# Kernel tuning notes

Measured on AMD Instinct MI355X. Metric: run time of the kernel, lower is better.

## Reference

```python
import jax, jax.numpy as jnp
import numpy as np

H = 16
D_MODEL = 1024
D_K = D_MODEL // H


def setup_inputs() -> dict:
    key = jax.random.key(0)
    ks = jax.random.split(key, 12)
    B, S = 2, 2048
    scale = 1.0 / np.sqrt(D_MODEL)
    inp = {
        "query": jax.random.normal(ks[0], (B, S, D_MODEL), jnp.float32),
        "key": jax.random.normal(ks[1], (B, S, D_MODEL), jnp.float32),
        "value": jax.random.normal(ks[2], (B, S, D_MODEL), jnp.float32),
        "mask": jnp.ones((B, 1, S), jnp.int32),
        "Wq": jax.random.normal(ks[3], (D_MODEL, D_MODEL), jnp.float32) * scale,
        "bq": jnp.zeros((D_MODEL,), jnp.float32),
        "Wk": jax.random.normal(ks[4], (D_MODEL, D_MODEL), jnp.float32) * scale,
        "bk": jnp.zeros((D_MODEL,), jnp.float32),
        "Wv": jax.random.normal(ks[5], (D_MODEL, D_MODEL), jnp.float32) * scale,
        "bv": jnp.zeros((D_MODEL,), jnp.float32),
        "Wo": jax.random.normal(ks[6], (D_MODEL, D_MODEL), jnp.float32) * scale,
        "bo": jnp.zeros((D_MODEL,), jnp.float32),
    }
    return inp


def reference(query, key, value, mask, Wq, bq, Wk, bk, Wv, bv, Wo, bo):
    B, S, _ = query.shape
    # QKV projections, split heads: [B, S, D] -> [B, H, S, d_k]
    def proj(x, W, b):
        y = x @ W.T + b
        return y.reshape(B, -1, H, D_K).transpose(0, 2, 1, 3)

    q = proj(query, Wq, bq)
    k = proj(key, Wk, bk)
    v = proj(value, Wv, bv)

    # scaled dot-product attention with full score matrix [B, H, Sq, Sk]
    scores = jnp.einsum("bhqd,bhkd->bhqk", q, k) / np.sqrt(D_K)
    m = mask[:, None, :, :]  # unsqueeze head dim: [B, 1, 1_or_S, S]
    scores = jnp.where(m == 0, jnp.float32(-1e9), scores)
    p_attn = jax.nn.softmax(scores, axis=-1)  # dropout p=0.0 (eval)
    x = jnp.einsum("bhqk,bhkd->bhqd", p_attn, v)

    # merge heads and output projection
    x = x.transpose(0, 2, 1, 3).reshape(B, -1, H * D_K)
    return x @ Wo.T + bo
```

## Files before the change

kernel.cpp:

```cpp
#include <hip/hip_runtime.h>
#include <hip/hip_bf16.h>
#include <stdint.h>

typedef unsigned short us;
typedef __bf16 bf8 __attribute__((ext_vector_type(8)));
typedef float  f4  __attribute__((ext_vector_type(4)));

typedef unsigned int __attribute__((address_space(1))) as1_uint;
typedef unsigned int __attribute__((address_space(3))) as3_uint;

__device__ __forceinline__ void async_ld16(const void* g, void* l) {
    __builtin_amdgcn_global_load_lds((as1_uint*)g, (as3_uint*)l, 16, 0, 0);
}

__device__ __forceinline__ us f2bf(float f) {
    __hip_bfloat16 h = __float2bfloat16(f);
    us u;
    __builtin_memcpy(&u, &h, 2);
    return u;
}

__global__ __launch_bounds__(256)
void convert_all(const float* __restrict__ s0, const float* __restrict__ s1,
                 const float* __restrict__ s2, const float* __restrict__ s3,
                 const float* __restrict__ s4, const float* __restrict__ s5,
                 const float* __restrict__ s6,
                 us* __restrict__ d0, us* __restrict__ d1, us* __restrict__ d2,
                 us* __restrict__ d3, us* __restrict__ d4, us* __restrict__ d5,
                 us* __restrict__ d6)
{
    size_t i4 = (((size_t)blockIdx.x * 256) + threadIdx.x) << 2;
    const float* src; us* dst; size_t off;
    if (i4 < ((size_t)3 << 22)) {
        unsigned seg = (unsigned)(i4 >> 22);
        off = i4 & (((size_t)1 << 22) - 1);
        src = seg == 0 ? s0 : (seg == 1 ? s1 : s2);
        dst = seg == 0 ? d0 : (seg == 1 ? d1 : d2);
    } else {
        size_t j = i4 - ((size_t)3 << 22);
        unsigned seg = (unsigned)(j >> 20);
        off = j & (((size_t)1 << 20) - 1);
        src = seg == 0 ? s3 : (seg == 1 ? s4 : (seg == 2 ? s5 : s6));
        dst = seg == 0 ? d3 : (seg == 1 ? d4 : (seg == 2 ? d5 : d6));
    }
    float4 f = *(const float4*)(src + off);
    ushort4 o;
    o.x = f2bf(f.x); o.y = f2bf(f.y); o.z = f2bf(f.z); o.w = f2bf(f.w);
    *(ushort4*)(dst + off) = o;
}

template<int MODE, int BN>
__device__ __forceinline__
void gemm_body(const us* __restrict__ A, const us* __restrict__ W,
               const float* __restrict__ bias, void* __restrict__ out,
               float scale, int bx, int by)
{
    __shared__ us lA[128 * 32];
    __shared__ us lB[BN * 32];

    const int tid  = threadIdx.x;
    const int wv   = tid >> 6;
    const int lane = tid & 63;
    const int l15  = lane & 15;
    const int quad = lane >> 4;
    const int kq   = quad << 3;
    const int cr   = quad << 2;
    const int srow = lane >> 2;
    const int scol = (lane & 3) << 3;
    const int m0   = by << 7;
    const int n0   = bx * BN;
    constexpr int MJ = (BN == 128) ? 4 : 2;
    const int wm = (BN == 128) ? ((wv >> 1) << 6) : (wv << 5);
    const int wn = (BN == 128) ? ((wv & 1) << 6) : 0;

    f4 acc[4][MJ];
    const f4 zero = {0.f, 0.f, 0.f, 0.f};
#pragma unroll
    for (int i = 0; i < 4; ++i)
#pragma unroll
        for (int j = 0; j < MJ; ++j) acc[i][j] = zero;

    for (int kt = 0; kt < 1024; kt += 32) {
#pragma unroll
        for (int s = 0; s < 2; ++s) {
            const int chunk = wv * 2 + s;
            const int row   = chunk * 16 + srow;
            async_ld16(A + (size_t)(m0 + row) * 1024 + kt + scol, &lA[chunk * 512]);
        }
        if (BN == 128) {
#pragma unroll
            for (int s = 0; s < 2; ++s) {
                const int chunk = wv * 2 + s;
                const int row   = chunk * 16 + srow;
                async_ld16(W + (size_t)(n0 + row) * 1024 + kt + scol, &lB[chunk * 512]);
            }
        } else {
            const int row = wv * 16 + srow;
            async_ld16(W + (size_t)(n0 + row) * 1024 + kt + scol, &lB[wv * 512]);
        }
        __syncthreads();

        bf8 wf[4], xf[MJ];
#pragma unroll
        for (int i = 0; i < 4; ++i)
            wf[i] = *(const bf8*)&lB[(wn + i * 16 + l15) * 32 + kq];
#pragma unroll
        for (int j = 0; j < MJ; ++j)
            xf[j] = *(const bf8*)&lA[(wm + j * 16 + l15) * 32 + kq];
#pragma unroll
        for (int i = 0; i < 4; ++i)
#pragma unroll
            for (int j = 0; j < MJ; ++j)
                acc[i][j] = __builtin_amdgcn_mfma_f32_16x16x32_bf16(wf[i], xf[j], acc[i][j], 0, 0, 0);
        __syncthreads();
    }

#pragma unroll
    for (int i = 0; i < 4; ++i) {
        const int gnb = n0 + wn + i * 16 + cr;
        const f4 bj = *(const f4*)&bias[gnb];
        if (MODE == 0) {
            us* o = (us*)out;
            const int hh = gnb >> 6, dd = gnb & 63;
#pragma unroll
            for (int j = 0; j < MJ; ++j) {
                const int gm = m0 + wm + j * 16 + l15;
                const int bb = gm >> 11, ss = gm & 2047;
                us hp[4];
#pragma unroll
                for (int r = 0; r < 4; ++r)
                    hp[r] = f2bf((acc[i][j][r] + bj[r]) * scale);
                uint2 w;
                w.x = (unsigned)hp[0] | ((unsigned)hp[1] << 16);
                w.y = (unsigned)hp[2] | ((unsigned)hp[3] << 16);
                *(uint2*)&o[(((size_t)(bb * 16 + hh) * 2048 + ss) << 6) + dd] = w;
            }
        } else {
            float* o = (float*)out;
#pragma unroll
            for (int j = 0; j < MJ; ++j) {
                const int gm = m0 + wm + j * 16 + l15;
                f4 v;
#pragma unroll
                for (int r = 0; r < 4; ++r) v[r] = acc[i][j][r] + bj[r];
                *(f4*)&o[((size_t)gm << 10) + gnb] = v;
            }
        }
    }
}

__global__ __launch_bounds__(256)
void gemm_qkv(const us* __restrict__ XQ, const us* __restrict__ XK,
              const us* __restrict__ XV,
              const us* __restrict__ WQ, const us* __restrict__ WK,
              const us* __restrict__ WV,
              const float* __restrict__ bq, const float* __restrict__ bk,
              const float* __restrict__ bv,
              us* __restrict__ QP, us* __restrict__ KP, us* __restrict__ VP)
{
    const int z = blockIdx.z;
    const us* A = z == 0 ? XQ : (z == 1 ? XK : XV);
    const us* W = z == 0 ? WQ : (z == 1 ? WK : WV);
    const float* b = z == 0 ? bq : (z == 1 ? bk : bv);
    us* o = z == 0 ? QP : (z == 1 ? KP : VP);
    const float scale = z == 0 ? 0.125f : 1.0f;
    gemm_body<0, 128>(A, W, b, o, scale, blockIdx.x, blockIdx.y);
}

__global__ __launch_bounds__(256)
void gemm_o(const us* __restrict__ A, const us* __restrict__ W,
            const float* __restrict__ bias, float* __restrict__ out)
{
    gemm_body<1, 64>(A, W, bias, out, 1.0f, blockIdx.x, blockIdx.y);
}

__global__ __launch_bounds__(256)
void flash_attn(const us* __restrict__ Qp, const us* __restrict__ Kp,
                const us* __restrict__ Vp, const int* __restrict__ maskp,
                us* __restrict__ ctx)
{
    __shared__ char smem[27136];
    us* lK    = (us*)smem;
    us* lVt   = (us*)(smem + 8192);
    us* lP    = (us*)(smem + 16384);
    float* lmask = (float*)(smem + 26624);
    float* liRed = (float*)(smem + 26880);
    float* red   = (float*)smem;

    const int tid  = threadIdx.x;
    const int wv   = tid >> 6;
    const int lane = tid & 63;
    const int l15  = lane & 15;
    const int quad = lane >> 4;
    const int cr   = quad << 2;
    const int qh   = wv & 1;
    const int kh   = wv >> 1;

    const int q0 = blockIdx.x << 6;
    const int h  = blockIdx.y;
    const int b  = blockIdx.z;

    const size_t headoff = ((size_t)(b * 16 + h)) << 17;
    const us* Qh = Qp + headoff;
    const us* Kh = Kp + headoff;
    const us* Vh = Vp + headoff;

    bf8 qf[2][2];
#pragma unroll
    for (int nt = 0; nt < 2; ++nt)
#pragma unroll
        for (int kb = 0; kb < 2; ++kb)
            qf[nt][kb] = *(const bf8*)(Qh + ((size_t)(q0 + qh * 32 + nt * 16 + l15) << 6)
                                          + kb * 32 + (quad << 3));

    const f4 zero = {0.f, 0.f, 0.f, 0.f};
    f4 of[4][2];
#pragma unroll
    for (int mt = 0; mt < 4; ++mt)
#pragma unroll
        for (int nt = 0; nt < 2; ++nt) of[mt][nt] = zero;
    float li[2] = {0.f, 0.f};

    us* lPw = lP + wv * (32 * 40);
    const int sc = tid & 7;
    const int sr = tid >> 3;
    const int ls = lane >> 3;

    for (int kt0 = 0; kt0 < 2048; kt0 += 64) {
        __syncthreads();

#pragma unroll
        for (int it = 0; it < 2; ++it) {
            const int r = sr + 32 * it;
            uint4 kv = *(const uint4*)(Kh + ((size_t)(kt0 + r) << 6) + sc * 8);
            *(uint4*)&lK[r * 64 + ((sc ^ ls) << 3)] = kv;
        }
#pragma unroll
        for (int it = 0; it < 2; ++it) {
            const int r = sr + 32 * it;
            uint4 vv = *(const uint4*)(Vh + ((size_t)(kt0 + r) << 6) + sc * 8);
            const us* u = (const us*)&vv;
            const int rhi = r >> 3;
#pragma unroll
            for (int jj = 0; jj < 8; ++jj) {
                const int d = sc * 8 + jj;
                const int p = (rhi ^ jj ^ sc) & 7;
                lVt[d * 64 + (p << 3) + ls] = u[jj];
            }
        }
        if (tid < 64)
            lmask[tid] = (maskp[((size_t)b << 11) + kt0 + tid] == 0) ? 0.0f : 1.0f;
        __syncthreads();

        f4 st[2][2];
#pragma unroll
        for (int mt2 = 0; mt2 < 2; ++mt2)
#pragma unroll
            for (int nt = 0; nt < 2; ++nt) st[mt2][nt] = zero;
#pragma unroll
        for (int mt2 = 0; mt2 < 2; ++mt2) {
            const int key = kh * 32 + mt2 * 16 + l15;
#pragma unroll
            for (int kb = 0; kb < 2; ++kb) {
                const int c = 4 * kb + quad;
                bf8 kf = *(const bf8*)&lK[key * 64 + ((c ^ (l15 & 7)) << 3)];
#pragma unroll
                for (int nt = 0; nt < 2; ++nt)
                    st[mt2][nt] = __builtin_amdgcn_mfma_f32_16x16x32_bf16(kf, qf[nt][kb], st[mt2][nt], 0, 0, 0);
            }
        }

        float rs[2] = {0.f, 0.f};
#pragma unroll
        for (int mt2 = 0; mt2 < 2; ++mt2) {
            const f4 mr = *(const f4*)&lmask[kh * 32 + mt2 * 16 + cr];
#pragma unroll
            for (int nt = 0; nt < 2; ++nt) {
                us hp[4];
#pragma unroll
                for (int r = 0; r < 4; ++r) {
                    const float pv = __expf(st[mt2][nt][r]) * mr[r];
                    rs[nt] += pv;
                    hp[r] = f2bf(pv);
                }
                uint2 w;
                w.x = (unsigned)hp[0] | ((unsigned)hp[1] << 16);
                w.y = (unsigned)hp[2] | ((unsigned)hp[3] << 16);
                *(uint2*)&lPw[(nt * 16 + l15) * 40 + mt2 * 16 + cr] = w;
            }
        }
#pragma unroll
        for (int nt = 0; nt < 2; ++nt) {
            float r2 = rs[nt];
            r2 += __shfl_xor(r2, 16, 64);
            r2 += __shfl_xor(r2, 32, 64);
            li[nt] += r2;
        }

        bf8 pf[2];
#pragma unroll
        for (int nt = 0; nt < 2; ++nt)
            pf[nt] = *(const bf8*)&lPw[(nt * 16 + l15) * 40 + (quad << 3)];
#pragma unroll
        for (int mt = 0; mt < 4; ++mt) {
            const int dd = mt * 16 + l15;
            const int c  = 4 * kh + quad;
            const int p  = (c ^ (dd & 7) ^ ((dd >> 3) & 7)) & 7;
            bf8 vf = *(const bf8*)&lVt[dd * 64 + (p << 3)];
#pragma unroll
            for (int nt = 0; nt < 2; ++nt)
                of[mt][nt] = __builtin_amdgcn_mfma_f32_16x16x32_bf16(vf, pf[nt], of[mt][nt], 0, 0, 0);
        }
    }

    __syncthreads();
    if (kh == 1) {
#pragma unroll
        for (int mt = 0; mt < 4; ++mt)
#pragma unroll
            for (int nt = 0; nt < 2; ++nt)
#pragma unroll
                for (int r = 0; r < 4; ++r)
                    red[qh * 2048 + (mt * 16 + cr + r) * 32 + nt * 16 + l15] = of[mt][nt][r];
        if (quad == 0) {
#pragma unroll
            for (int nt = 0; nt < 2; ++nt)
                liRed[qh * 32 + nt * 16 + l15] = li[nt];
        }
    }
    __syncthreads();
    if (kh == 0) {
#pragma unroll
        for (int mt = 0; mt < 4; ++mt)
#pragma unroll
            for (int nt = 0; nt < 2; ++nt)
#pragma unroll
                for (int r = 0; r < 4; ++r)
                    of[mt][nt][r] += red[qh * 2048 + (mt * 16 + cr + r) * 32 + nt * 16 + l15];
#pragma unroll
        for (int nt = 0; nt < 2; ++nt) {
            const float linv = 1.0f / (li[nt] + liRed[qh * 32 + nt * 16 + l15]);
            const int tok = q0 + qh * 32 + nt * 16 + l15;
            const size_t rowb = (((size_t)b * 2048 + tok) << 10) + (h << 6);
#pragma unroll
            for (int mt = 0; mt < 4; ++mt) {
                us hp[4];
#pragma unroll
                for (int r = 0; r < 4; ++r) hp[r] = f2bf(of[mt][nt][r] * linv);
                uint2 w;
                w.x = (unsigned)hp[0] | ((unsigned)hp[1] << 16);
                w.y = (unsigned)hp[2] | ((unsigned)hp[3] << 16);
                *(uint2*)&ctx[rowb + mt * 16 + cr] = w;
            }
        }
    }
}

extern "C" void kernel_launch(void* const* d_in, const int* in_sizes, int n_in,
                              void* d_out, int out_size, void* d_ws, size_t ws_size,
                              hipStream_t stream)
{
    const float* q    = (const float*)d_in[0];
    const float* k    = (const float*)d_in[1];
    const float* v    = (const float*)d_in[2];
    const int*   mask = (const int*)d_in[3];
    const float* Wq   = (const float*)d_in[4];
    const float* bq   = (const float*)d_in[5];
    const float* Wk   = (const float*)d_in[6];
    const float* bk   = (const float*)d_in[7];
    const float* Wv   = (const float*)d_in[8];
    const float* bv   = (const float*)d_in[9];
    const float* Wo   = (const float*)d_in[10];
    const float* bo   = (const float*)d_in[11];
    float* out = (float*)d_out;

    us* ws  = (us*)d_ws;
    us* XQ  = ws;
    us* XK  = ws + 4194304;
    us* XV  = ws + 8388608;
    us* WQb = ws + 12582912;
    us* WKb = ws + 13631488;
    us* WVb = ws + 14680064;
    us* WOb = ws + 15728640;
    us* QP  = ws + 16777216;
    us* KP  = ws + 20971520;
    us* VP  = ws + 25165824;
    us* CTX = XQ;

    convert_all<<<16384, 256, 0, stream>>>(q, k, v, Wq, Wk, Wv, Wo,
                                           XQ, XK, XV, WQb, WKb, WVb, WOb);
    gemm_qkv<<<dim3(8, 32, 3), 256, 0, stream>>>(XQ, XK, XV, WQb, WKb, WVb,
                                                 bq, bk, bv, QP, KP, VP);
    flash_attn<<<dim3(32, 16, 2), 256, 0, stream>>>(QP, KP, VP, mask, CTX);
    gemm_o<<<dim3(16, 32), 256, 0, stream>>>(CTX, WOb, bo, out);
}
```

Before: 272.2 us.

## Emit transposed V from projection GEMM and restructure flash attention per-wave tiling

The V projection is now computed as W·Xᵀ and written directly in a head-major transposed layout, so the attention kernel copies V tiles into LDS with plain vector stores instead of a scalar transpose scatter. The attention kernel moves to 128 threads where each wave owns 64 query rows across the full key tile, which removes the cross-wave output reduction through LDS and raises MFMA work per LDS load. The Q scale now includes log2(e) so a raw exp2 builtin replaces __expf. Fewer, larger blocks reduce total waves in flight, and the higher per-wave register use may lower occupancy.

```diff
diff --git a/kernel.cpp b/kernel.cpp
--- a/kernel.cpp
+++ b/kernel.cpp
@@ -19,6 +19,16 @@
     __builtin_memcpy(&u, &h, 2);
     return u;
 }
+
+__device__ __forceinline__ float fexp2(float x) {
+#if __has_builtin(__builtin_amdgcn_exp2f)
+    return __builtin_amdgcn_exp2f(x);
+#else
+    return exp2f(x);
+#endif
+}
+
+#define SCALE_Q 0.18033688011112042f
 
 __global__ __launch_bounds__(256)
 void convert_all(const float* __restrict__ s0, const float* __restrict__ s1,
@@ -115,6 +125,29 @@
         __syncthreads();
     }
 
+    if (MODE == 2) {
+        us* o = (us*)out;
+#pragma unroll
+        for (int j = 0; j < MJ; ++j) {
+            const int f = m0 + wm + j * 16 + l15;
+            const float bf_ = bias[f];
+            const int hh = f >> 6, dd = f & 63;
+#pragma unroll
+            for (int i = 0; i < 4; ++i) {
+                const int tokb = n0 + wn + i * 16 + cr;
+                const int bb = tokb >> 11, ss = tokb & 2047;
+                us hp[4];
+#pragma unroll
+                for (int r = 0; r < 4; ++r) hp[r] = f2bf(acc[i][j][r] + bf_);
+                uint2 w;
+                w.x = (unsigned)hp[0] | ((unsigned)hp[1] << 16);
+                w.y = (unsigned)hp[2] | ((unsigned)hp[3] << 16);
+                *(uint2*)&o[((size_t)((bb * 16 + hh) * 64 + dd) << 11) + ss] = w;
+            }
+        }
+        return;
+    }
+
 #pragma unroll
     for (int i = 0; i < 4; ++i) {
         const int gnb = n0 + wn + i * 16 + cr;
@@ -156,14 +189,18 @@
               const us* __restrict__ WV,
               const float* __restrict__ bq, const float* __restrict__ bk,
               const float* __restrict__ bv,
-              us* __restrict__ QP, us* __restrict__ KP, us* __restrict__ VP)
+              us* __restrict__ QP, us* __restrict__ KP, us* __restrict__ VT)
 {
     const int z = blockIdx.z;
-    const us* A = z == 0 ? XQ : (z == 1 ? XK : XV);
-    const us* W = z == 0 ? WQ : (z == 1 ? WK : WV);
-    const float* b = z == 0 ? bq : (z == 1 ? bk : bv);
-    us* o = z == 0 ? QP : (z == 1 ? KP : VP);
-    const float scale = z == 0 ? 0.125f : 1.0f;
+    if (z == 2) {
+        gemm_body<2, 128>(WV, XV, bv, VT, 1.0f, blockIdx.y, blockIdx.x);
+        return;
+    }
+    const us* A = z == 0 ? XQ : XK;
+    const us* W = z == 0 ? WQ : WK;
+    const float* b = z == 0 ? bq : bk;
+    us* o = z == 0 ? QP : KP;
+    const float scale = z == 0 ? SCALE_Q : 1.0f;
     gemm_body<0, 128>(A, W, b, o, scale, blockIdx.x, blockIdx.y);
 }
 
@@ -174,18 +211,15 @@
     gemm_body<1, 64>(A, W, bias, out, 1.0f, blockIdx.x, blockIdx.y);
 }
 
-__global__ __launch_bounds__(256)
+__global__ __launch_bounds__(128)
 void flash_attn(const us* __restrict__ Qp, const us* __restrict__ Kp,
-                const us* __restrict__ Vp, const int* __restrict__ maskp,
+                const us* __restrict__ Vtp, const int* __restrict__ maskp,
                 us* __restrict__ ctx)
 {
-    __shared__ char smem[27136];
-    us* lK    = (us*)smem;
-    us* lVt   = (us*)(smem + 8192);
-    us* lP    = (us*)(smem + 16384);
-    float* lmask = (float*)(smem + 26624);
-    float* liRed = (float*)(smem + 26880);
-    float* red   = (float*)smem;
+    __shared__ us lK[64 * 64];
+    __shared__ us lVt[64 * 64];
+    __shared__ us lP[2 * 64 * 72];
+    __shared__ float lmask[64];
 
     const int tid  = threadIdx.x;
     const int wv   = tid >> 6;
@@ -193,165 +227,120 @@
     const int l15  = lane & 15;
     const int quad = lane >> 4;
     const int cr   = quad << 2;
-    const int qh   = wv & 1;
-    const int kh   = wv >> 1;
-
-    const int q0 = blockIdx.x << 6;
+    const int l7   = l15 & 7;
+
+    const int q0 = blockIdx.x << 7;
     const int h  = blockIdx.y;
     const int b  = blockIdx.z;
 
     const size_t headoff = ((size_t)(b * 16 + h)) << 17;
-    const us* Qh = Qp + headoff;
-    const us* Kh = Kp + headoff;
-    const us* Vh = Vp + headoff;
-
-    bf8 qf[2][2];
-#pragma unroll
-    for (int nt = 0; nt < 2; ++nt)
+    const us* Qh  = Qp  + headoff;
+    const us* Kh  = Kp  + headoff;
+    const us* Vth = Vtp + headoff;
+
+    bf8 qf[4][2];
+#pragma unroll
+    for (int nt = 0; nt < 4; ++nt)
 #pragma unroll
         for (int kb = 0; kb < 2; ++kb)
-            qf[nt][kb] = *(const bf8*)(Qh + ((size_t)(q0 + qh * 32 + nt * 16 + l15) << 6)
+            qf[nt][kb] = *(const bf8*)(Qh + ((size_t)(q0 + wv * 64 + nt * 16 + l15) << 6)
                                           + kb * 32 + (quad << 3));
 
     const f4 zero = {0.f, 0.f, 0.f, 0.f};
-    f4 of[4][2];
-#pragma unroll
-    for (int mt = 0; mt < 4; ++mt)
-#pragma unroll
-        for (int nt = 0; nt < 2; ++nt) of[mt][nt] = zero;
-    float li[2] = {0.f, 0.f};
-
-    us* lPw = lP + wv * (32 * 40);
+    f4 of[4][4];
+#pragma unroll
+    for (int dt = 0; dt < 4; ++dt)
+#pragma unroll
+        for (int nt = 0; nt < 4; ++nt) of[dt][nt] = zero;
+    float li[4] = {0.f, 0.f, 0.f, 0.f};
+
+    us* lPw = lP + wv * (64 * 72);
+
+    const int sr = tid >> 3;
     const int sc = tid & 7;
-    const int sr = tid >> 3;
-    const int ls = lane >> 3;
 
     for (int kt0 = 0; kt0 < 2048; kt0 += 64) {
         __syncthreads();
 
 #pragma unroll
-        for (int it = 0; it < 2; ++it) {
-            const int r = sr + 32 * it;
+        for (int it = 0; it < 4; ++it) {
+            const int r = sr + 16 * it;
+            const int sw = (sc ^ (r & 7)) << 3;
             uint4 kv = *(const uint4*)(Kh + ((size_t)(kt0 + r) << 6) + sc * 8);
-            *(uint4*)&lK[r * 64 + ((sc ^ ls) << 3)] = kv;
-        }
-#pragma unroll
-        for (int it = 0; it < 2; ++it) {
-            const int r = sr + 32 * it;
-            uint4 vv = *(const uint4*)(Vh + ((size_t)(kt0 + r) << 6) + sc * 8);
-            const us* u = (const us*)&vv;
-            const int rhi = r >> 3;
-#pragma unroll
-            for (int jj = 0; jj < 8; ++jj) {
-                const int d = sc * 8 + jj;
-                const int p = (rhi ^ jj ^ sc) & 7;
-                lVt[d * 64 + (p << 3) + ls] = u[jj];
-            }
+            *(uint4*)&lK[(r << 6) + sw] = kv;
+            uint4 vv = *(const uint4*)(Vth + (size_t)r * 2048 + kt0 + sc * 8);
+            *(uint4*)&lVt[(r << 6) + sw] = vv;
         }
         if (tid < 64)
             lmask[tid] = (maskp[((size_t)b << 11) + kt0 + tid] == 0) ? 0.0f : 1.0f;
         __syncthreads();
 
-        f4 st[2][2];
-#pragma unroll
-        for (int mt2 = 0; mt2 < 2; ++mt2)
-#pragma unroll
-            for (int nt = 0; nt < 2; ++nt) st[mt2][nt] = zero;
-#pragma unroll
-        for (int mt2 = 0; mt2 < 2; ++mt2) {
-            const int key = kh * 32 + mt2 * 16 + l15;
-#pragma unroll
-            for (int kb = 0; kb < 2; ++kb) {
-                const int c = 4 * kb + quad;
-                bf8 kf = *(const bf8*)&lK[key * 64 + ((c ^ (l15 & 7)) << 3)];
-#pragma unroll
-                for (int nt = 0; nt < 2; ++nt)
-                    st[mt2][nt] = __builtin_amdgcn_mfma_f32_16x16x32_bf16(kf, qf[nt][kb], st[mt2][nt], 0, 0, 0);
-            }
-        }
-
-        float rs[2] = {0.f, 0.f};
-#pragma unroll
-        for (int mt2 = 0; mt2 < 2; ++mt2) {
-            const f4 mr = *(const f4*)&lmask[kh * 32 + mt2 * 16 + cr];
-#pragma unroll
-            for (int nt = 0; nt < 2; ++nt) {
+        float rs[4] = {0.f, 0.f, 0.f, 0.f};
+#pragma unroll
+        for (int kt = 0; kt < 4; ++kt) {
+            const int krow = (kt * 16 + l15) << 6;
+            bf8 kf0 = *(const bf8*)&lK[krow + ((quad ^ l7) << 3)];
+            bf8 kf1 = *(const bf8*)&lK[krow + (((4 + quad) ^ l7) << 3)];
+            f4 st[4];
+#pragma unroll
+            for (int nt = 0; nt < 4; ++nt) {
+                st[nt] = __builtin_amdgcn_mfma_f32_16x16x32_bf16(kf0, qf[nt][0], zero, 0, 0, 0);
+                st[nt] = __builtin_amdgcn_mfma_f32_16x16x32_bf16(kf1, qf[nt][1], st[nt], 0, 0, 0);
+            }
+            const f4 mr = *(const f4*)&lmask[kt * 16 + cr];
+#pragma unroll
+            for (int nt = 0; nt < 4; ++nt) {
                 us hp[4];
 #pragma unroll
                 for (int r = 0; r < 4; ++r) {
-                    const float pv = __expf(st[mt2][nt][r]) * mr[r];
-                    rs[nt] += pv;
-                    hp[r] = f2bf(pv);
+                    const float p = fexp2(st[nt][r]) * mr[r];
+                    rs[nt] += p;
+                    hp[r] = f2bf(p);
                 }
                 uint2 w;
                 w.x = (unsigned)hp[0] | ((unsigned)hp[1] << 16);
                 w.y = (unsigned)hp[2] | ((unsigned)hp[3] << 16);
-                *(uint2*)&lPw[(nt * 16 + l15) * 40 + mt2 * 16 + cr] = w;
-            }
-        }
-#pragma unroll
-        for (int nt = 0; nt < 2; ++nt) {
+                *(uint2*)&lPw[(nt * 16 + l15) * 72 + kt * 16 + cr] = w;
+            }
+        }
+#pragma unroll
+        for (int nt = 0; nt < 4; ++nt) {
             float r2 = rs[nt];
             r2 += __shfl_xor(r2, 16, 64);
             r2 += __shfl_xor(r2, 32, 64);
             li[nt] += r2;
         }
 
-        bf8 pf[2];
-#pragma unroll
-        for (int nt = 0; nt < 2; ++nt)
-            pf[nt] = *(const bf8*)&lPw[(nt * 16 + l15) * 40 + (quad << 3)];
-#pragma unroll
-        for (int mt = 0; mt < 4; ++mt) {
-            const int dd = mt * 16 + l15;
-            const int c  = 4 * kh + quad;
-            const int p  = (c ^ (dd & 7) ^ ((dd >> 3) & 7)) & 7;
-            bf8 vf = *(const bf8*)&lVt[dd * 64 + (p << 3)];
-#pragma unroll
-            for (int nt = 0; nt < 2; ++nt)
-                of[mt][nt] = __builtin_amdgcn_mfma_f32_16x16x32_bf16(vf, pf[nt], of[mt][nt], 0, 0, 0);
-        }
-    }
-
-    __syncthreads();
-    if (kh == 1) {
-#pragma unroll
-        for (int mt = 0; mt < 4; ++mt)
-#pragma unroll
-            for (int nt = 0; nt < 2; ++nt)
-#pragma unroll
-                for (int r = 0; r < 4; ++r)
-                    red[qh * 2048 + (mt * 16 + cr + r) * 32 + nt * 16 + l15] = of[mt][nt][r];
-        if (quad == 0) {
-#pragma unroll
-            for (int nt = 0; nt < 2; ++nt)
-                liRed[qh * 32 + nt * 16 + l15] = li[nt];
-        }
-    }
-    __syncthreads();
-    if (kh == 0) {
-#pragma unroll
-        for (int mt = 0; mt < 4; ++mt)
-#pragma unroll
-            for (int nt = 0; nt < 2; ++nt)
-#pragma unroll
-                for (int r = 0; r < 4; ++r)
-                    of[mt][nt][r] += red[qh * 2048 + (mt * 16 + cr + r) * 32 + nt * 16 + l15];
-#pragma unroll
-        for (int nt = 0; nt < 2; ++nt) {
-            const float linv = 1.0f / (li[nt] + liRed[qh * 32 + nt * 16 + l15]);
-            const int tok = q0 + qh * 32 + nt * 16 + l15;
-            const size_t rowb = (((size_t)b * 2048 + tok) << 10) + (h << 6);
-#pragma unroll
-            for (int mt = 0; mt < 4; ++mt) {
-                us hp[4];
-#pragma unroll
-                for (int r = 0; r < 4; ++r) hp[r] = f2bf(of[mt][nt][r] * linv);
-                uint2 w;
-                w.x = (unsigned)hp[0] | ((unsigned)hp[1] << 16);
-                w.y = (unsigned)hp[2] | ((unsigned)hp[3] << 16);
-                *(uint2*)&ctx[rowb + mt * 16 + cr] = w;
-            }
+#pragma unroll
+        for (int kb = 0; kb < 2; ++kb) {
+            bf8 pfr[4];
+#pragma unroll
+            for (int nt = 0; nt < 4; ++nt)
+                pfr[nt] = *(const bf8*)&lPw[(nt * 16 + l15) * 72 + kb * 32 + (quad << 3)];
+#pragma unroll
+            for (int dt = 0; dt < 4; ++dt) {
+                bf8 vf = *(const bf8*)&lVt[((dt * 16 + l15) << 6) + (((kb * 4 + quad) ^ l7) << 3)];
+#pragma unroll
+                for (int nt = 0; nt < 4; ++nt)
+                    of[dt][nt] = __builtin_amdgcn_mfma_f32_16x16x32_bf16(vf, pfr[nt], of[dt][nt], 0, 0, 0);
+            }
+        }
+    }
+
+#pragma unroll
+    for (int nt = 0; nt < 4; ++nt) {
+        const float linv = 1.0f / li[nt];
+        const int tok = q0 + wv * 64 + nt * 16 + l15;
+        const size_t rowb = (((size_t)(b * 2048 + tok)) << 10) + (h << 6);
+#pragma unroll
+        for (int dt = 0; dt < 4; ++dt) {
+            us hp[4];
+#pragma unroll
+            for (int r = 0; r < 4; ++r) hp[r] = f2bf(of[dt][nt][r] * linv);
+            uint2 w;
+            w.x = (unsigned)hp[0] | ((unsigned)hp[1] << 16);
+            w.y = (unsigned)hp[2] | ((unsigned)hp[3] << 16);
+            *(uint2*)&ctx[rowb + dt * 16 + cr] = w;
         }
     }
 }
@@ -384,13 +373,13 @@
     us* WOb = ws + 15728640;
     us* QP  = ws + 16777216;
     us* KP  = ws + 20971520;
-    us* VP  = ws + 25165824;
+    us* VT  = ws + 25165824;
     us* CTX = XQ;
 
     convert_all<<<16384, 256, 0, stream>>>(q, k, v, Wq, Wk, Wv, Wo,
                                            XQ, XK, XV, WQb, WKb, WVb, WOb);
     gemm_qkv<<<dim3(8, 32, 3), 256, 0, stream>>>(XQ, XK, XV, WQb, WKb, WVb,
-                                                 bq, bk, bv, QP, KP, VP);
-    flash_attn<<<dim3(32, 16, 2), 256, 0, stream>>>(QP, KP, VP, mask, CTX);
+                                                 bq, bk, bv, QP, KP, VT);
+    flash_attn<<<dim3(16, 16, 2), 128, 0, stream>>>(QP, KP, VT, mask, CTX);
     gemm_o<<<dim3(16, 32), 256, 0, stream>>>(CTX, WOb, bo, out);
 }
```

After: 257.0 us. 5.6% less time.
